# Performance work log

Hardware: AMD Instinct MI355X
Metric: run time of the kernel (lower is better)

## Reference

```python
import jax, jax.numpy as jnp
import numpy as np

N = 50000   # nodes
E = 800000  # edges (avg degree 16)
D = 128     # node feature dim
DE = 16     # edge feature dim
H = 128     # MLP hidden dim
MSG_IN = 2 * D + DE + 1  # src feat + dst feat + edge feat + squared distance


def setup_inputs() -> dict:
    key = jax.random.key(0)
    ks = jax.random.split(key, 10)
    def wmat(k, shp):
        return jax.random.normal(k, shp, jnp.float32) * 0.05
    return {
        "f": jax.random.normal(ks[0], (N, D), jnp.float32),
        "x": jax.random.normal(ks[1], (N, 3), jnp.float32),
        "w": jax.random.normal(ks[2], (E, DE), jnp.float32),
        "src": jax.random.randint(ks[3], (E,), 0, N),
        "dst": jax.random.randint(ks[4], (E,), 0, N),
        "Wm1": wmat(ks[5], (MSG_IN, H)), "bm1": jnp.zeros((H,), jnp.float32),
        "Wm2": wmat(ks[6], (H, D)),      "bm2": jnp.zeros((D,), jnp.float32),
        "Wu1": wmat(ks[7], (D, H)),      "bu1": jnp.zeros((H,), jnp.float32),
        "Wu2": wmat(ks[8], (H, D)),      "bu2": jnp.zeros((D,), jnp.float32),
    }


def reference(f, x, w, src, dst, Wm1, bm1, Wm2, bm2, Wu1, bu1, Wu2, bu2):
    # message: gather endpoint features, squared distance, concat, MLP  [E, D]
    sqd = jnp.sum((x[src] - x[dst]) ** 2, axis=-1, keepdims=True)  # [E, 1]
    msg_in = jnp.concatenate([f[src], f[dst], w, sqd], axis=-1)    # [E, MSG_IN]
    m = jnp.dot(jax.nn.relu(jnp.dot(msg_in, Wm1) + bm1), Wm2) + bm2  # [E, D]
    # reduce: sum messages at destination nodes (DGL fn.sum)
    m_sum = jax.ops.segment_sum(m, dst, num_segments=N)             # [N, D]
    # update: node MLP on m_sum + f
    h = m_sum + f
    f_new = jnp.dot(jax.nn.relu(jnp.dot(h, Wu1) + bu1), Wu2) + bu2  # [N, D]
    return f_new
```

## Files before the change

kernel.cpp:

```cpp
#include <hip/hip_runtime.h>
#include <hip/hip_fp8.h>

#define D 128
#define HD 128
#define DE 16
#define MSG_IN 273
#define EB 64
#define NT 256
#define KP1 288
#define NCH2 4
#define NB 32
#define HID_PAD 132
#define CH8 (4 * EB * 64)
#define LDS1 (4 * EB * 64 + EB * 32)
#define OB 8192
#define OC 24576

typedef __attribute__((ext_vector_type(8))) short short8v;
typedef __attribute__((ext_vector_type(4))) float f32x4;
typedef unsigned short ushort_t;
typedef unsigned char uchar_t;

#define GLOAD_LDS16(gp, lp) \
    __builtin_amdgcn_global_load_lds((const __attribute__((address_space(1))) unsigned int*)(gp), \
                                     (__attribute__((address_space(3))) unsigned int*)(lp), 16, 0, 0)

__device__ __forceinline__ unsigned short f2bf(float v) {
    unsigned int u = __builtin_bit_cast(unsigned int, v);
    u += 0x7fffu + ((u >> 16) & 1u);
    return (unsigned short)(u >> 16);
}
__device__ __forceinline__ float bf2f(ushort_t u) {
    return __builtin_bit_cast(float, (unsigned int)u << 16);
}
__device__ __forceinline__ unsigned int cvt_pk_bf16(float lo, float hi) {
    unsigned int r;
    asm("v_cvt_pk_bf16_f32 %0, %1, %2" : "=v"(r) : "v"(lo), "v"(hi));
    return r;
}
__device__ __forceinline__ uchar_t f8e(float v) {
    __hip_fp8_e4m3 t(v);
    return (uchar_t)t.__x;
}
__device__ __forceinline__ float f8d(unsigned b) {
    unsigned t = ((b & 0x7fu) << 20) | ((b & 0x80u) << 24);
    return __builtin_bit_cast(float, t) * 0x1p120f;
}

__global__ void fused_pre_kernel(const float* __restrict__ Wm1, const float* __restrict__ Wm2,
                                 const float* __restrict__ Wu1, const float* __restrict__ Wu2,
                                 ushort_t* __restrict__ W1p, ushort_t* __restrict__ W2p,
                                 ushort_t* __restrict__ Wu1p, ushort_t* __restrict__ Wu2p,
                                 const float* __restrict__ w, ushort_t* __restrict__ wbf,
                                 const int* __restrict__ dst, int* __restrict__ cnt,
                                 int nw8, int E) {
    const int gid    = blockIdx.x * 256 + threadIdx.x;
    const int stride = gridDim.x * 256;
    const int rp1 = 128 * KP1;
    const int rp2 = rp1 + HD * D;
    const int rp_elems = rp2 + 2 * HD * D;
    for (int i = gid; i < rp_elems; i += stride) {
        if (i < rp1) {
            int n = i / KP1, k = i % KP1;
            W1p[i] = f2bf((k < MSG_IN) ? Wm1[(size_t)k * HD + n] : 0.f);
        } else if (i < rp2) {
            int i2 = i - rp1;
            int n = i2 / HD, k = i2 % HD;
            W2p[i2] = f2bf(Wm2[(size_t)k * D + n]);
        } else {
            int i2 = (i - rp2);
            const bool second = i2 >= HD * D;
            if (second) i2 -= HD * D;
            int n = i2 / HD, k = i2 % HD;
            if (second) Wu2p[i2] = f2bf(Wu2[(size_t)k * D + n]);
            else        Wu1p[i2] = f2bf(Wu1[(size_t)k * HD + n]);
        }
    }
    for (int i = gid; i < nw8; i += stride) {
        float4 v0 = *(const float4*)(w + (size_t)i * 8);
        float4 v1 = *(const float4*)(w + (size_t)i * 8 + 4);
        union { ushort_t us[8]; short8v v; } pk;
        pk.us[0] = f2bf(v0.x); pk.us[1] = f2bf(v0.y);
        pk.us[2] = f2bf(v0.z); pk.us[3] = f2bf(v0.w);
        pk.us[4] = f2bf(v1.x); pk.us[5] = f2bf(v1.y);
        pk.us[6] = f2bf(v1.z); pk.us[7] = f2bf(v1.w);
        *(short8v*)(wbf + (size_t)i * 8) = pk.v;
    }
    for (int i = gid; i < E; i += stride) atomicAdd(&cnt[dst[i]], 1);
}

__global__ __launch_bounds__(1024) void scan_kernel(const int* __restrict__ cnt,
                                                    int* __restrict__ roff,
                                                    int* __restrict__ cursor, int Nn) {
    __shared__ int wsum[16];
    const int t = threadIdx.x, l = t & 63, wid = t >> 6;
    int running = 0;
    for (int base = 0; base < Nn; base += 4096) {
        const int i0 = base + t * 4;
        int v0 = 0, v1 = 0, v2 = 0, v3 = 0;
        if (i0 + 3 < Nn) {
            int4 v = *(const int4*)(cnt + i0);
            v0 = v.x; v1 = v.y; v2 = v.z; v3 = v.w;
        } else {
            if (i0 + 0 < Nn) v0 = cnt[i0 + 0];
            if (i0 + 1 < Nn) v1 = cnt[i0 + 1];
            if (i0 + 2 < Nn) v2 = cnt[i0 + 2];
        }
        const int vsum = v0 + v1 + v2 + v3;
        int s = vsum;
        #pragma unroll
        for (int off = 1; off < 64; off <<= 1) {
            int u = __shfl_up(s, off, 64);
            if (l >= off) s += u;
        }
        if (l == 63) wsum[wid] = s;
        __syncthreads();
        if (wid == 0 && l < 16) {
            int xv = wsum[l];
            #pragma unroll
            for (int off = 1; off < 16; off <<= 1) {
                int u = __shfl_up(xv, off, 64);
                if (l >= off) xv += u;
            }
            wsum[l] = xv;
        }
        __syncthreads();
        const int prev  = (wid > 0) ? wsum[wid - 1] : 0;
        const int total = wsum[15];
        int ex = running + prev + (s - vsum);
        if (i0 + 0 < Nn) { roff[i0 + 0] = ex; cursor[i0 + 0] = ex; } ex += v0;
        if (i0 + 1 < Nn) { roff[i0 + 1] = ex; cursor[i0 + 1] = ex; } ex += v1;
        if (i0 + 2 < Nn) { roff[i0 + 2] = ex; cursor[i0 + 2] = ex; } ex += v2;
        if (i0 + 3 < Nn) { roff[i0 + 3] = ex; cursor[i0 + 3] = ex; }
        running += total;
        __syncthreads();
    }
}

__global__ void scatter_kernel(const int* __restrict__ dst, int* cursor,
                               const int* __restrict__ roff, const int* __restrict__ cnt,
                               int* __restrict__ perm, int* __restrict__ sdst,
                               float* __restrict__ mh, int E, int Nn) {
    const int gid    = blockIdx.x * 256 + threadIdx.x;
    const int stride = gridDim.x * 256;
    for (int i = gid; i < E; i += stride) {
        int d = dst[i];
        int s = atomicAdd(&cursor[d], 1);
        perm[s] = i;
        sdst[s] = d;
    }
    for (int n = gid; n < Nn; n += stride) {
        const int c = cnt[n];
        const int r = roff[n];
        const bool need0 = (c == 0) || (r / EB != (r + c - 1) / EB);
        if (need0) {
            float4 z = {0.f, 0.f, 0.f, 0.f};
            float* p = mh + (size_t)n * D;
            #pragma unroll
            for (int k = 0; k < 32; ++k) *(float4*)(p + k * 4) = z;
        }
    }
}

__global__ __launch_bounds__(NT, 4) void ab_kernel(
    const float* __restrict__ f,
    const ushort_t* __restrict__ W1p,
    uchar_t* __restrict__ Af, ushort_t* __restrict__ Bf16, int Nn)
{
    __shared__ __align__(16) ushort_t lds[2 * 64 * 64];

    const int t    = threadIdx.x;
    const int lane = t & 63;
    const int wv   = t >> 6;
    const int col  = lane & 15;
    const int g    = lane >> 4;
    const int n0   = blockIdx.x * 64;

    #pragma unroll
    for (int it = 0; it < 4; ++it) {
        const int gidx = it * 256 + t;
        const int row  = gidx >> 4;
        const int gr   = gidx & 15;
        const int pair = gr >> 3, s = gr & 7;
        const int sP   = s ^ (row & 7);
        const int gn   = min(n0 + row, Nn - 1);
        const size_t off = (size_t)gn * D + gr * 8;
        float4 v0 = *(const float4*)(f + off);
        float4 v1 = *(const float4*)(f + off + 4);
        union { ushort_t us[8]; short8v v; } pk;
        pk.us[0] = f2bf(v0.x); pk.us[1] = f2bf(v0.y);
        pk.us[2] = f2bf(v0.z); pk.us[3] = f2bf(v0.w);
        pk.us[4] = f2bf(v1.x); pk.us[5] = f2bf(v1.y);
        pk.us[6] = f2bf(v1.z); pk.us[7] = f2bf(v1.w);
        *(short8v*)&lds[(pair * 64 + row) * 64 + sP * 8] = pk.v;
    }
    __syncthreads();

    const bool even = (col & 1) == 0;
    #pragma unroll
    for (int half = 0; half < 2; ++half) {
        f32x4 acc[4][2];
        #pragma unroll
        for (int rt = 0; rt < 4; ++rt) {
            acc[rt][0] = (f32x4){0.f, 0.f, 0.f, 0.f};
            acc[rt][1] = (f32x4){0.f, 0.f, 0.f, 0.f};
        }
        const int kbase = half * 128;
        #pragma unroll
        for (int c = 0; c < 4; ++c) {
            short8v b0 = *(const short8v*)&W1p[(size_t)(wv * 32 + col) * KP1 + kbase + c * 32 + g * 8];
            short8v b1 = *(const short8v*)&W1p[(size_t)(wv * 32 + 16 + col) * KP1 + kbase + c * 32 + g * 8];
            short8v a[4];
            #pragma unroll
            for (int rt = 0; rt < 4; ++rt) {
                const int row = rt * 16 + col;
                const int sP = (((c & 1) << 2) + g) ^ (row & 7);
                a[rt] = *(const short8v*)&lds[((c >> 1) * 64 + row) * 64 + sP * 8];
            }
            #pragma unroll
            for (int rt = 0; rt < 4; ++rt) {
                acc[rt][0] = __builtin_amdgcn_mfma_f32_16x16x32_bf16(a[rt], b0, acc[rt][0], 0, 0, 0);
                acc[rt][1] = __builtin_amdgcn_mfma_f32_16x16x32_bf16(a[rt], b1, acc[rt][1], 0, 0, 0);
            }
        }
        #pragma unroll
        for (int rt = 0; rt < 4; ++rt)
            #pragma unroll
            for (int j = 0; j < 2; ++j)
                #pragma unroll
                for (int r = 0; r < 4; ++r) {
                    const int row = rt * 16 + g * 4 + r;
                    const int gn = n0 + row;
                    float v  = acc[rt][j][r];
                    float vn = __shfl_xor(v, 1, 64);
                    if (even && gn < Nn) {
                        const int ca = wv * 32 + j * 16 + col;
                        if (half == 0) {
                            ushort_t pk = (ushort_t)f8e(v) | ((ushort_t)f8e(vn) << 8);
                            *(ushort_t*)(Af + (size_t)gn * D + ca) = pk;
                        } else {
                            *(unsigned int*)(Bf16 + (size_t)gn * D + ca) = cvt_pk_bf16(v, vn);
                        }
                    }
                }
    }
}

__global__ __launch_bounds__(NT, 4) void edge_lin_kernel(
    const uchar_t* __restrict__ Af, const ushort_t* __restrict__ Bf16,
    const float* __restrict__ x, const ushort_t* __restrict__ wbf,
    const int* __restrict__ src,
    const int* __restrict__ perm, const int* __restrict__ sdst,
    const ushort_t* __restrict__ W1p, const float* __restrict__ bm1,
    float* __restrict__ mh, int E)
{
    __shared__ __align__(16) uchar_t lds8[28672];
    __shared__ int s_rid[EB];
    __shared__ int s_dgs[EB];

    const int t    = threadIdx.x;
    const int lane = t & 63;
    const int wv   = t >> 6;
    const int e0   = blockIdx.x * EB;
    const int nvalid = min(EB, E - e0);

    const int myd  = (e0 + lane < E) ? sdst[e0 + lane] : -1;
    const int prevd = (e0 > 0) ? sdst[e0 - 1] : -2;
    const int nextd = (e0 + EB < E) ? sdst[e0 + EB] : -2;

    const int dprev_l = __shfl_up(myd, 1, 64);
    const bool head = (lane == 0) || (myd != dprev_l);
    const unsigned long long mask = __ballot(head && (lane < nvalid));
    const unsigned long long le = (lane == 63) ? ~0ull : ((1ull << (lane + 1)) - 1ull);
    const int rid = (int)__popcll(mask & le) - 1;
    const int ndist = (int)__popcll(mask);
    s_rid[lane] = (rid < 0) ? 0 : rid;
    if (head && lane < nvalid) s_dgs[rid] = myd;

    {
        const int el8 = lane >> 3;
        const int s   = lane & 7;
        const int sl  = s ^ el8;
        const int slA = min(e0 + wv * 16 + el8,     E - 1);
        const int slB = min(e0 + wv * 16 + 8 + el8, E - 1);
        const int nsA = src[perm[slA]];
        const int nsB = src[perm[slB]];
        GLOAD_LDS16(Af + (size_t)nsA * D + sl * 16, &lds8[(wv * 16    ) * 128]);
        GLOAD_LDS16(Af + (size_t)nsB * D + sl * 16, &lds8[(wv * 16 + 8) * 128]);
    }
    {
        const int ntask = ndist * 16;
        for (int idx = t; idx < ntask; idx += NT) {
            const int rowr = idx >> 4;
            const int gr   = idx & 15;
            const int dg   = s_dgs[rowr];
            uint4 v = *(const uint4*)(Bf16 + (size_t)dg * D + gr * 8);
            const int phys = gr ^ (rowr & 15);
            *(uint4*)&lds8[OB + rowr * 256 + phys * 16] = v;
        }
    }
    {
        const int el = lane >> 2, q = lane & 3;
        const int qp = q ^ (el & 3);
        const int slot = e0 + wv * 16 + el;
        const bool ok = slot < E;
        const int sc = min(slot, E - 1);
        const int ge = perm[sc];
        union { ushort_t us[8]; short8v v; } pk;
        #pragma unroll
        for (int j = 0; j < 8; ++j) pk.us[j] = 0;
        if (ok) {
            if (q < 2) {
                pk.v = *(const short8v*)(wbf + (size_t)ge * DE + q * 8);
            } else if (q == 2) {
                const int ns = src[ge], nd = sdst[sc];
                float dx = x[ns*3+0] - x[nd*3+0];
                float dy = x[ns*3+1] - x[nd*3+1];
                float dz = x[ns*3+2] - x[nd*3+2];
                pk.us[0] = f2bf(dx*dx + dy*dy + dz*dz);
            }
        }
        *(short8v*)&lds8[OC + (wv * 16 + el) * 64 + qp * 16] = pk.v;
    }

    const int col = lane & 15;
    const int g   = lane >> 4;

    short8v bc0 = *(const short8v*)&W1p[(size_t)(wv * 32 + col) * KP1 + 256 + g * 8];
    short8v bc1 = *(const short8v*)&W1p[(size_t)(wv * 32 + 16 + col) * KP1 + 256 + g * 8];

    __syncthreads();

    f32x4 acc[4][2];
    {
        float bv0 = bm1[wv * 32 + col];
        float bv1 = bm1[wv * 32 + 16 + col];
        #pragma unroll
        for (int rt = 0; rt < 4; ++rt) {
            acc[rt][0] = (f32x4){bv0, bv0, bv0, bv0};
            acc[rt][1] = (f32x4){bv1, bv1, bv1, bv1};
        }
    }
    #pragma unroll
    for (int rt = 0; rt < 4; ++rt) {
        const int row = rt * 16 + col;
        const int sP8 = g ^ (row & 3);
        short8v a = *(const short8v*)&lds8[OC + row * 64 + sP8 * 16];
        acc[rt][0] = __builtin_amdgcn_mfma_f32_16x16x32_bf16(a, bc0, acc[rt][0], 0, 0, 0);
        acc[rt][1] = __builtin_amdgcn_mfma_f32_16x16x32_bf16(a, bc1, acc[rt][1], 0, 0, 0);
    }

    float h[4][2][4];
    #pragma unroll
    for (int rt = 0; rt < 4; ++rt) {
        #pragma unroll
        for (int r = 0; r < 4; ++r) {
            const int row = rt * 16 + g * 4 + r;
            const int rd  = s_rid[row];
            #pragma unroll
            for (int j = 0; j < 2; ++j) {
                const int ca = wv * 32 + j * 16 + col;
                const uchar_t ab = lds8[row * 128 + (((ca >> 4) ^ (row & 7)) << 4) + (ca & 15)];
                const ushort_t bb = *(const ushort_t*)&lds8[OB + rd * 256 + (((ca >> 3) ^ (rd & 15)) << 4) + (ca & 7) * 2];
                h[rt][j][r] = fmaxf(acc[rt][j][r] + f8d(ab) + bf2f(bb), 0.f);
            }
        }
    }

    float qs[4][2];
    #pragma unroll
    for (int rt = 0; rt < 4; ++rt) {
        qs[rt][0] = (h[rt][0][0] + h[rt][0][1]) + (h[rt][0][2] + h[rt][0][3]);
        qs[rt][1] = (h[rt][1][0] + h[rt][1][1]) + (h[rt][1][2] + h[rt][1][3]);
    }
    unsigned long long rem = mask;
    while (rem) {
        const int beg = (int)__builtin_ctzll(rem);
        rem &= rem - 1;
        const int end = rem ? (int)__builtin_ctzll(rem) : nvalid;
        const int dg  = __shfl(myd, beg, 64);

        float s0 = 0.f, s1 = 0.f;
        #pragma unroll
        for (int rt = 0; rt < 4; ++rt) {
            const int qb = rt * 16 + g * 4;
            const int lo = max(qb, beg);
            const int hi = min(qb + 4, end);
            if (lo < hi) {
                if (lo == qb && hi == qb + 4) {
                    s0 += qs[rt][0]; s1 += qs[rt][1];
                } else {
                    #pragma unroll
                    for (int r = 0; r < 4; ++r) {
                        const int sl = qb + r;
                        if (sl >= beg && sl < end) {
                            s0 += h[rt][0][r]; s1 += h[rt][1][r];
                        }
                    }
                }
            }
        }
        s0 += __shfl_xor(s0, 16, 64); s0 += __shfl_xor(s0, 32, 64);
        s1 += __shfl_xor(s1, 16, 64); s1 += __shfl_xor(s1, 32, 64);
        if (g == 0) {
            const bool bnd = (beg == 0 && dg == prevd) || (end == nvalid && dg == nextd);
            float* p = mh + (size_t)dg * D + wv * 32 + col;
            if (bnd) { atomicAdd(p, s0); atomicAdd(p + 16, s1); }
            else     { p[0] = s0; p[16] = s1; }
        }
    }
}

__global__ __launch_bounds__(NT, 4) void node_fused_kernel(
    const float* __restrict__ f, const float* __restrict__ mh,
    const int* __restrict__ cnt,
    const ushort_t* __restrict__ W2p, const float* __restrict__ bm2,
    const ushort_t* __restrict__ Wu1p, const float* __restrict__ bu1,
    const ushort_t* __restrict__ Wu2p, const float* __restrict__ bu2,
    float* __restrict__ out, int Nn)
{
    __shared__ __align__(16) ushort_t lds[2 * 64 * 64];
    __shared__ int s_cnt[64];

    const int t    = threadIdx.x;
    const int lane = t & 63;
    const int wv   = t >> 6;
    const int col  = lane & 15;
    const int g    = lane >> 4;
    const int n0   = blockIdx.x * 64;

    if (t < 64) s_cnt[t] = (n0 + t < Nn) ? cnt[n0 + t] : 0;

    #pragma unroll
    for (int it = 0; it < 4; ++it) {
        const int gidx = it * 256 + t;
        const int row  = gidx >> 4;
        const int gr   = gidx & 15;
        const int pair = gr >> 3, s = gr & 7;
        const int sP   = s ^ (row & 7);
        const int gn   = n0 + row;
        union { ushort_t us[8]; short8v v; } pk;
        if (gn < Nn) {
            const size_t off = (size_t)gn * D + gr * 8;
            float4 m0 = *(const float4*)(mh + off);
            float4 m1 = *(const float4*)(mh + off + 4);
            pk.us[0] = f2bf(m0.x); pk.us[1] = f2bf(m0.y);
            pk.us[2] = f2bf(m0.z); pk.us[3] = f2bf(m0.w);
            pk.us[4] = f2bf(m1.x); pk.us[5] = f2bf(m1.y);
            pk.us[6] = f2bf(m1.z); pk.us[7] = f2bf(m1.w);
        } else {
            #pragma unroll
            for (int j = 0; j < 8; ++j) pk.us[j] = 0;
        }
        *(short8v*)&lds[(pair * 64 + row) * 64 + sP * 8] = pk.v;
    }
    __syncthreads();

    f32x4 acc[4][2];
    {
        const float bv0 = bm2[wv * 32 + col];
        const float bv1 = bm2[wv * 32 + 16 + col];
        #pragma unroll
        for (int rt = 0; rt < 4; ++rt)
            #pragma unroll
            for (int r = 0; r < 4; ++r) {
                const float cn = (float)s_cnt[rt * 16 + g * 4 + r];
                acc[rt][0][r] = cn * bv0;
                acc[rt][1][r] = cn * bv1;
            }
    }
    #pragma unroll
    for (int c = 0; c < 4; ++c) {
        short8v b0 = *(const short8v*)&W2p[(size_t)(wv * 32 + col) * HD + c * 32 + g * 8];
        short8v b1 = *(const short8v*)&W2p[(size_t)(wv * 32 + 16 + col) * HD + c * 32 + g * 8];
        short8v a[4];
        #pragma unroll
        for (int rt = 0; rt < 4; ++rt) {
            const int row = rt * 16 + col;
            const int sP = (((c & 1) << 2) + g) ^ (row & 7);
            a[rt] = *(const short8v*)&lds[((c >> 1) * 64 + row) * 64 + sP * 8];
        }
        #pragma unroll
        for (int rt = 0; rt < 4; ++rt) {
            acc[rt][0] = __builtin_amdgcn_mfma_f32_16x16x32_bf16(a[rt], b0, acc[rt][0], 0, 0, 0);
            acc[rt][1] = __builtin_amdgcn_mfma_f32_16x16x32_bf16(a[rt], b1, acc[rt][1], 0, 0, 0);
        }
    }
    __syncthreads();

    const int ph = wv >> 1;
    #pragma unroll
    for (int rt = 0; rt < 4; ++rt)
        #pragma unroll
        for (int r = 0; r < 4; ++r) {
            const int row = rt * 16 + g * 4 + r;
            const int gn = n0 + row;
            #pragma unroll
            for (int j = 0; j < 2; ++j) {
                const int ca = wv * 32 + j * 16 + col;
                float v = 0.f;
                if (gn < Nn) v = acc[rt][j][r] + f[(size_t)gn * D + ca];
                unsigned int pk2 = cvt_pk_bf16(v, v);
                const int sH = (((wv & 1) << 2) + j * 2 + (col >> 3)) ^ (row & 7);
                lds[(ph * 64 + row) * 64 + sH * 8 + (col & 7)] = (ushort_t)pk2;
            }
        }
    __syncthreads();

    const size_t wrow0 = (size_t)(wv * 32 + col) * HD;
    const size_t wrow1 = (size_t)(wv * 32 + 16 + col) * HD;
    f32x4 acc1[4][2];
    {
        float bv0 = bu1[wv * 32 + col];
        float bv1 = bu1[wv * 32 + 16 + col];
        #pragma unroll
        for (int rt = 0; rt < 4; ++rt) {
            acc1[rt][0] = (f32x4){bv0, bv0, bv0, bv0};
            acc1[rt][1] = (f32x4){bv1, bv1, bv1, bv1};
        }
    }
    #pragma unroll
    for (int c = 0; c < 4; ++c) {
        short8v b0 = *(const short8v*)&Wu1p[wrow0 + c * 32 + g * 8];
        short8v b1 = *(const short8v*)&Wu1p[wrow1 + c * 32 + g * 8];
        short8v a[4];
        #pragma unroll
        for (int rt = 0; rt < 4; ++rt) {
            const int row = rt * 16 + col;
            const int sP = (((c & 1) << 2) + g) ^ (row & 7);
            a[rt] = *(const short8v*)&lds[((c >> 1) * 64 + row) * 64 + sP * 8];
        }
        #pragma unroll
        for (int rt = 0; rt < 4; ++rt) {
            acc1[rt][0] = __builtin_amdgcn_mfma_f32_16x16x32_bf16(a[rt], b0, acc1[rt][0], 0, 0, 0);
            acc1[rt][1] = __builtin_amdgcn_mfma_f32_16x16x32_bf16(a[rt], b1, acc1[rt][1], 0, 0, 0);
        }
    }
    __syncthreads();

    #pragma unroll
    for (int rt = 0; rt < 4; ++rt)
        #pragma unroll
        for (int j = 0; j < 2; ++j)
            #pragma unroll
            for (int r = 0; r < 4; ++r) {
                const int row = rt * 16 + g * 4 + r;
                float v = fmaxf(acc1[rt][j][r], 0.f);
                unsigned int pk2 = cvt_pk_bf16(v, v);
                const int sH = (((wv & 1) << 2) + j * 2 + (col >> 3)) ^ (row & 7);
                lds[(ph * 64 + row) * 64 + sH * 8 + (col & 7)] = (ushort_t)pk2;
            }
    __syncthreads();

    f32x4 acc2[4][2];
    {
        float bv0 = bu2[wv * 32 + col];
        float bv1 = bu2[wv * 32 + 16 + col];
        #pragma unroll
        for (int rt = 0; rt < 4; ++rt) {
            acc2[rt][0] = (f32x4){bv0, bv0, bv0, bv0};
            acc2[rt][1] = (f32x4){bv1, bv1, bv1, bv1};
        }
    }
    #pragma unroll
    for (int c = 0; c < 4; ++c) {
        short8v b0 = *(const short8v*)&Wu2p[wrow0 + c * 32 + g * 8];
        short8v b1 = *(const short8v*)&Wu2p[wrow1 + c * 32 + g * 8];
        short8v a[4];
        #pragma unroll
        for (int rt = 0; rt < 4; ++rt) {
            const int row = rt * 16 + col;
            const int sP = (((c & 1) << 2) + g) ^ (row & 7);
            a[rt] = *(const short8v*)&lds[((c >> 1) * 64 + row) * 64 + sP * 8];
        }
        #pragma unroll
        for (int rt = 0; rt < 4; ++rt) {
            acc2[rt][0] = __builtin_amdgcn_mfma_f32_16x16x32_bf16(a[rt], b0, acc2[rt][0], 0, 0, 0);
            acc2[rt][1] = __builtin_amdgcn_mfma_f32_16x16x32_bf16(a[rt], b1, acc2[rt][1], 0, 0, 0);
        }
    }

    #pragma unroll
    for (int rt = 0; rt < 4; ++rt)
        #pragma unroll
        for (int r = 0; r < 4; ++r) {
            const int row = rt * 16 + g * 4 + r;
            const int gn = n0 + row;
            if (gn < Nn) {
                out[(size_t)gn * D + wv * 32 + col]      = acc2[rt][0][r];
                out[(size_t)gn * D + wv * 32 + 16 + col] = acc2[rt][1][r];
            }
        }
}


__global__ void repack_kernel(const float* __restrict__ Wm1, const float* __restrict__ Wm2,
                              ushort_t* __restrict__ W1p, ushort_t* __restrict__ W2p) {
    int idx = blockIdx.x * 256 + threadIdx.x;
    const int n1 = 128 * KP1;
    if (idx < n1) {
        int n = idx / KP1, k = idx % KP1;
        W1p[idx] = f2bf((k < MSG_IN) ? Wm1[(size_t)k * HD + n] : 0.f);
    } else {
        int i2 = idx - n1;
        if (i2 < HD * D) {
            int n = i2 / HD, k = i2 % HD;
            W2p[i2] = f2bf(Wm2[(size_t)k * D + n]);
        }
    }
}

__global__ void fconv_kernel(const float* __restrict__ f, ushort_t* __restrict__ fb, int n8) {
    int i = blockIdx.x * 256 + threadIdx.x;
    if (i < n8) {
        float4 v0 = *(const float4*)(f + (size_t)i * 8);
        float4 v1 = *(const float4*)(f + (size_t)i * 8 + 4);
        union { ushort_t us[8]; short8v v; } pk;
        pk.us[0] = f2bf(v0.x); pk.us[1] = f2bf(v0.y);
        pk.us[2] = f2bf(v0.z); pk.us[3] = f2bf(v0.w);
        pk.us[4] = f2bf(v1.x); pk.us[5] = f2bf(v1.y);
        pk.us[6] = f2bf(v1.z); pk.us[7] = f2bf(v1.w);
        *(short8v*)(fb + (size_t)i * 8) = pk.v;
    }
}

__global__ __launch_bounds__(NT, 4) void edge_mfma_kernel(
    const ushort_t* __restrict__ fbf, const float* __restrict__ x,
    const float* __restrict__ w, const int* __restrict__ src,
    const int* __restrict__ dst,
    const ushort_t* __restrict__ W1p, const float* __restrict__ bm1,
    const ushort_t* __restrict__ W2p, const float* __restrict__ bm2,
    ushort_t* msum, int E)
{
    __shared__ __align__(16) ushort_t lds[LDS1];
    __shared__ int s_dst[EB];

    const int t    = threadIdx.x;
    const int lane = t & 63;
    const int wv   = t >> 6;
    const int e0   = blockIdx.x * EB;

    if (t < EB) s_dst[t] = (e0 + t < E) ? dst[e0 + t] : 0;
    {
        const int el8 = lane >> 3;
        const int s   = lane & 7;
        const int sl  = s ^ el8;
        const int geA = min(e0 + wv * 16 + el8,     E - 1);
        const int geB = min(e0 + wv * 16 + 8 + el8, E - 1);
        const int nsA = src[geA], ndA = dst[geA];
        const int nsB = src[geB], ndB = dst[geB];
        #pragma unroll
        for (int p = 0; p < 4; ++p) {
            const int n0 = (p < 2) ? nsA : ndA;
            const int n1 = (p < 2) ? nsB : ndB;
            const ushort_t* g0 = fbf + (size_t)n0 * D + (p & 1) * 64 + sl * 8;
            const ushort_t* g1 = fbf + (size_t)n1 * D + (p & 1) * 64 + sl * 8;
            GLOAD_LDS16(g0, &lds[(p * EB + wv * 16    ) * 64]);
            GLOAD_LDS16(g1, &lds[(p * EB + wv * 16 + 8) * 64]);
        }
    }
    {
        const int el = lane >> 2, q = lane & 3;
        const int qp = q ^ (el & 3);
        const int ge = e0 + wv * 16 + el;
        const bool ok = ge < E;
        const int gc = min(ge, E - 1);
        union { ushort_t us[8]; short8v v; } pk;
        #pragma unroll
        for (int j = 0; j < 8; ++j) pk.us[j] = 0;
        if (ok) {
            if (q < 2) {
                float4 w0 = *(const float4*)(w + (size_t)gc * DE + q * 8);
                float4 w1 = *(const float4*)(w + (size_t)gc * DE + q * 8 + 4);
                pk.us[0] = f2bf(w0.x); pk.us[1] = f2bf(w0.y);
                pk.us[2] = f2bf(w0.z); pk.us[3] = f2bf(w0.w);
                pk.us[4] = f2bf(w1.x); pk.us[5] = f2bf(w1.y);
                pk.us[6] = f2bf(w1.z); pk.us[7] = f2bf(w1.w);
            } else if (q == 2) {
                const int ns = src[gc], nd = dst[gc];
                float dx = x[ns*3+0] - x[nd*3+0];
                float dy = x[ns*3+1] - x[nd*3+1];
                float dz = x[ns*3+2] - x[nd*3+2];
                pk.us[0] = f2bf(dx*dx + dy*dy + dz*dz);
            }
        }
        *(short8v*)&lds[CH8 + (wv * 16 + el) * 32 + qp * 8] = pk.v;
    }

    const int col = lane & 15;
    const int g   = lane >> 4;
    const size_t wrow0 = (size_t)(wv * 32 + col) * KP1;
    const size_t wrow1 = (size_t)(wv * 32 + 16 + col) * KP1;
    short8v nb0 = *(const short8v*)&W1p[wrow0 + g * 8];
    short8v nb1 = *(const short8v*)&W1p[wrow1 + g * 8];
    __syncthreads();

    f32x4 acc[4][2];
    {
        float bv0 = bm1[wv * 32 + col];
        float bv1 = bm1[wv * 32 + 16 + col];
        #pragma unroll
        for (int rt = 0; rt < 4; ++rt) {
            acc[rt][0] = (f32x4){bv0, bv0, bv0, bv0};
            acc[rt][1] = (f32x4){bv1, bv1, bv1, bv1};
        }
    }
    #pragma unroll
    for (int c = 0; c < 9; ++c) {
        short8v b0 = nb0, b1 = nb1;
        if (c + 1 < 9) {
            nb0 = *(const short8v*)&W1p[wrow0 + (c + 1) * 32 + g * 8];
            nb1 = *(const short8v*)&W1p[wrow1 + (c + 1) * 32 + g * 8];
        }
        short8v a[4];
        #pragma unroll
        for (int rt = 0; rt < 4; ++rt) {
            const int row = rt * 16 + col;
            if (c < 8) {
                const int sP = (((c & 1) << 2) + g) ^ (row & 7);
                a[rt] = *(const short8v*)&lds[((c >> 1) * EB + row) * 64 + sP * 8];
            } else {
                const int sP = g ^ (row & 3);
                a[rt] = *(const short8v*)&lds[CH8 + row * 32 + sP * 8];
            }
        }
        #pragma unroll
        for (int rt = 0; rt < 4; ++rt) {
            acc[rt][0] = __builtin_amdgcn_mfma_f32_16x16x32_bf16(a[rt], b0, acc[rt][0], 0, 0, 0);
            acc[rt][1] = __builtin_amdgcn_mfma_f32_16x16x32_bf16(a[rt], b1, acc[rt][1], 0, 0, 0);
        }
    }
    __syncthreads();

    const int ph = wv >> 1;
    #pragma unroll
    for (int rt = 0; rt < 4; ++rt)
        #pragma unroll
        for (int j = 0; j < 2; ++j)
            #pragma unroll
            for (int r = 0; r < 4; ++r) {
                const int row = rt * 16 + g * 4 + r;
                float v = fmaxf(acc[rt][j][r], 0.f);
                unsigned int pk2 = cvt_pk_bf16(v, v);
                const int sH = (((wv & 1) << 2) + j * 2 + (col >> 3)) ^ (row & 7);
                lds[(ph * EB + row) * 64 + sH * 8 + (col & 7)] = (ushort_t)pk2;
            }
    __syncthreads();

    const size_t w2r0 = (size_t)(wv * 32 + col) * HD;
    const size_t w2r1 = (size_t)(wv * 32 + 16 + col) * HD;
    short8v m0 = *(const short8v*)&W2p[w2r0 + g * 8];
    short8v m1 = *(const short8v*)&W2p[w2r1 + g * 8];
    f32x4 acc2[4][2];
    {
        float bv0 = bm2[wv * 32 + col];
        float bv1 = bm2[wv * 32 + 16 + col];
        #pragma unroll
        for (int rt = 0; rt < 4; ++rt) {
            acc2[rt][0] = (f32x4){bv0, bv0, bv0, bv0};
            acc2[rt][1] = (f32x4){bv1, bv1, bv1, bv1};
        }
    }
    #pragma unroll
    for (int c = 0; c < NCH2; ++c) {
        short8v b0 = m0, b1 = m1;
        if (c + 1 < NCH2) {
            m0 = *(const short8v*)&W2p[w2r0 + (c + 1) * 32 + g * 8];
            m1 = *(const short8v*)&W2p[w2r1 + (c + 1) * 32 + g * 8];
        }
        short8v a[4];
        #pragma unroll
        for (int rt = 0; rt < 4; ++rt) {
            const int row = rt * 16 + col;
            const int sP = (((c & 1) << 2) + g) ^ (row & 7);
            a[rt] = *(const short8v*)&lds[((c >> 1) * EB + row) * 64 + sP * 8];
        }
        #pragma unroll
        for (int rt = 0; rt < 4; ++rt) {
            acc2[rt][0] = __builtin_amdgcn_mfma_f32_16x16x32_bf16(a[rt], b0, acc2[rt][0], 0, 0, 0);
            acc2[rt][1] = __builtin_amdgcn_mfma_f32_16x16x32_bf16(a[rt], b1, acc2[rt][1], 0, 0, 0);
        }
    }

    const bool even = (col & 1) == 0;
    #pragma unroll
    for (int rt = 0; rt < 4; ++rt)
        #pragma unroll
        for (int r = 0; r < 4; ++r) {
            const int e  = rt * 16 + g * 4 + r;
            const int ge = e0 + e;
            const int dg = s_dst[e];
            #pragma unroll
            for (int j = 0; j < 2; ++j) {
                float v  = acc2[rt][j][r];
                float vn = __shfl_xor(v, 1, 64);
                if (even && ge < E) {
                    unsigned int pk2 = cvt_pk_bf16(v, vn);
                    ushort_t* p = msum + (size_t)dg * D + wv * 32 + j * 16 + col;
                    asm volatile("global_atomic_pk_add_bf16 %0, %1, off"
                                 :: "v"(p), "v"(pk2) : "memory");
                }
            }
        }
}

template<bool MB16>
__global__ __launch_bounds__(NT, 4) void node_kernel(
    const float* __restrict__ f, const void* __restrict__ msum_v,
    const float* __restrict__ Wu1, const float* __restrict__ bu1,
    const float* __restrict__ Wu2, const float* __restrict__ bu2,
    float* out, int Nn)
{
    __shared__ __align__(16) float hin[NB][HID_PAD];
    __shared__ __align__(16) float hid[NB][HID_PAD];
    const int t  = threadIdx.x;
    const int n0 = blockIdx.x * NB;
    const int nn = min(NB, Nn - n0);

    {
        #pragma unroll
        for (int it = 0; it < 4; ++it) {
            const int idx = it * 1024 + t * 4;
            const int e   = idx >> 7;
            const int cb  = idx & 127;
            if (e < nn) {
                const size_t off = (size_t)(n0 + e) * D + cb;
                float4 mv;
                if (MB16) {
                    uint2 pk = *(const uint2*)((const ushort_t*)msum_v + off);
                    mv.x = bf2f((ushort_t)(pk.x & 0xffffu));
                    mv.y = bf2f((ushort_t)(pk.x >> 16));
                    mv.z = bf2f((ushort_t)(pk.y & 0xffffu));
                    mv.w = bf2f((ushort_t)(pk.y >> 16));
                } else {
                    mv = *(const float4*)((const float*)msum_v + off);
                }
                float4 fv = *(const float4*)&f[off];
                float4 o = {mv.x + fv.x, mv.y + fv.y, mv.z + fv.z, mv.w + fv.w};
                *(float4*)&hin[e][cb] = o;
            }
        }
    }
    __syncthreads();

    const int tc = t & 15, te2 = (t >> 4) * 2, c0 = tc * 8;
    float a1[2][8];
    #pragma unroll
    for (int c = 0; c < 8; ++c) { float bv = bu1[c0 + c]; a1[0][c] = bv; a1[1][c] = bv; }
    for (int i = 0; i < D; i += 4) {
        float m0[4], m1[4];
        *(float4*)m0 = *(const float4*)&hin[te2][i];
        *(float4*)m1 = *(const float4*)&hin[te2 + 1][i];
        #pragma unroll
        for (int r = 0; r < 4; ++r) {
            float wr[8];
            *(float4*)&wr[0] = *(const float4*)(Wu1 + (size_t)(i + r) * HD + c0);
            *(float4*)&wr[4] = *(const float4*)(Wu1 + (size_t)(i + r) * HD + c0 + 4);
            #pragma unroll
            for (int c = 0; c < 8; ++c) { a1[0][c] += m0[r]*wr[c]; a1[1][c] += m1[r]*wr[c]; }
        }
    }
    #pragma unroll
    for (int j = 0; j < 2; ++j) {
        float v[8];
        #pragma unroll
        for (int c = 0; c < 8; ++c) v[c] = fmaxf(a1[j][c], 0.f);
        *(float4*)&hid[te2 + j][c0] = *(float4*)&v[0];
        *(float4*)&hid[te2 + j][c0 + 4] = *(float4*)&v[4];
    }
    __syncthreads();
    float a2[2][8];
    #pragma unroll
    for (int c = 0; c < 8; ++c) { float bv = bu2[c0 + c]; a2[0][c] = bv; a2[1][c] = bv; }
    for (int h = 0; h < HD; h += 4) {
        float m0[4], m1[4];
        *(float4*)m0 = *(const float4*)&hid[te2][h];
        *(float4*)m1 = *(const float4*)&hid[te2 + 1][h];
        #pragma unroll
        for (int r = 0; r < 4; ++r) {
            float wr[8];
            *(float4*)&wr[0] = *(const float4*)(Wu2 + (size_t)(h + r) * D + c0);
            *(float4*)&wr[4] = *(const float4*)(Wu2 + (size_t)(h + r) * D + c0 + 4);
            #pragma unroll
            for (int c = 0; c < 8; ++c) { a2[0][c] += m0[r]*wr[c]; a2[1][c] += m1[r]*wr[c]; }
        }
    }
    #pragma unroll
    for (int j = 0; j < 2; ++j) {
        int e = te2 + j, gn = n0 + e;
        if (e < nn) {
            *(float4*)(out + (size_t)gn * D + c0) = *(float4*)&a2[j][0];
            *(float4*)(out + (size_t)gn * D + c0 + 4) = *(float4*)&a2[j][4];
        }
    }
}

extern "C" void kernel_launch(void* const* d_in, const int* in_sizes, int n_in,
                              void* d_out, int out_size, void* d_ws, size_t ws_size,
                              hipStream_t stream) {
    const float* f   = (const float*)d_in[0];
    const float* x   = (const float*)d_in[1];
    const float* w   = (const float*)d_in[2];
    const int*   src = (const int*)d_in[3];
    const int*   dst = (const int*)d_in[4];
    const float* Wm1 = (const float*)d_in[5];
    const float* bm1 = (const float*)d_in[6];
    const float* Wm2 = (const float*)d_in[7];
    const float* bm2 = (const float*)d_in[8];
    const float* Wu1 = (const float*)d_in[9];
    const float* bu1 = (const float*)d_in[10];
    const float* Wu2 = (const float*)d_in[11];
    const float* bu2 = (const float*)d_in[12];

    const int Nn = in_sizes[0] / D;
    const int E  = in_sizes[3];

    const size_t wbytes  = (size_t)(128 * KP1 + HD * D) * sizeof(ushort_t);
    const size_t wubytes = (size_t)(2 * HD * D) * sizeof(ushort_t);
    auto align512 = [](size_t v) { return (v + 511) & ~(size_t)511; };
    char* wsb = (char*)d_ws;

    size_t off = 0;
    const size_t o_w    = off; off = align512(off + wbytes);
    const size_t o_wu   = off; off = align512(off + wubytes);
    const size_t o_wbf  = off; off = align512(off + (size_t)E * DE * 2);
    const size_t o_af   = off; off = align512(off + (size_t)Nn * D);
    const size_t o_bf16 = off; off = align512(off + (size_t)Nn * D * 2);
    const size_t o_cnt  = off; off = align512(off + (size_t)Nn * 4);
    const size_t o_roff = off; off = align512(off + (size_t)Nn * 4);
    const size_t o_cur  = off; off = align512(off + (size_t)Nn * 4);
    const size_t o_perm = off; off = align512(off + (size_t)E * 4);
    const size_t o_sdst = off; off = align512(off + (size_t)E * 4);
    const size_t o_mh   = off; off = align512(off + (size_t)Nn * D * 4);
    const size_t primary_total = off;

    if (ws_size >= primary_total) {
        ushort_t* W1p  = (ushort_t*)(wsb + o_w);
        ushort_t* W2p  = W1p + 128 * KP1;
        ushort_t* Wu1p = (ushort_t*)(wsb + o_wu);
        ushort_t* Wu2p = Wu1p + HD * D;
        ushort_t* wbf  = (ushort_t*)(wsb + o_wbf);
        uchar_t*  Af   = (uchar_t*)(wsb + o_af);
        ushort_t* Bf16 = (ushort_t*)(wsb + o_bf16);
        int* cnt       = (int*)(wsb + o_cnt);
        int* roff      = (int*)(wsb + o_roff);
        int* cursor    = (int*)(wsb + o_cur);
        int* perm      = (int*)(wsb + o_perm);
        int* sdst      = (int*)(wsb + o_sdst);
        float* mh      = (float*)(wsb + o_mh);

        const int nw8 = E * DE / 8;
        const int ntiles = (E + EB - 1) / EB;
        const int nblk   = (Nn + 63) / 64;
        hipMemsetAsync(cnt, 0, (size_t)Nn * 4, stream);
        fused_pre_kernel<<<dim3(1024), dim3(256), 0, stream>>>(
            Wm1, Wm2, Wu1, Wu2, W1p, W2p, Wu1p, Wu2p, w, wbf, dst, cnt, nw8, E);
        scan_kernel<<<dim3(1), dim3(1024), 0, stream>>>(cnt, roff, cursor, Nn);
        scatter_kernel<<<dim3((E + 255) / 256), dim3(256), 0, stream>>>(
            dst, cursor, roff, cnt, perm, sdst, mh, E, Nn);
        ab_kernel<<<dim3(nblk), dim3(NT), 0, stream>>>(f, W1p, Af, Bf16, Nn);
        edge_lin_kernel<<<dim3(ntiles), dim3(NT), 0, stream>>>(
            Af, Bf16, x, wbf, src, perm, sdst, W1p, bm1, mh, E);
        node_fused_kernel<<<dim3(nblk), dim3(NT), 0, stream>>>(
            f, mh, cnt, W2p, bm2, Wu1p, bu1, Wu2p, bu2, (float*)d_out, Nn);
        return;
    }

    size_t off2 = 0;
    const size_t p_w  = off2; off2 = align512(off2 + wbytes);
    const size_t p_fb = off2; off2 = align512(off2 + (size_t)Nn * D * 2);
    const size_t p_ms = off2; off2 = align512(off2 + (size_t)Nn * D * 2);
    if (ws_size >= off2) {
        ushort_t* W1p  = (ushort_t*)(wsb + p_w);
        ushort_t* W2p  = W1p + 128 * KP1;
        ushort_t* fbf  = (ushort_t*)(wsb + p_fb);
        ushort_t* msum = (ushort_t*)(wsb + p_ms);
        const int rp_elems = 128 * KP1 + HD * D;
        hipMemsetAsync(msum, 0, (size_t)Nn * D * 2, stream);
        repack_kernel<<<dim3((rp_elems + 255) / 256), dim3(256), 0, stream>>>(Wm1, Wm2, W1p, W2p);
        const int n8 = Nn * D / 8;
        fconv_kernel<<<dim3((n8 + 255) / 256), dim3(256), 0, stream>>>(f, fbf, n8);
        edge_mfma_kernel<<<dim3((E + EB - 1) / EB), dim3(NT), 0, stream>>>(
            fbf, x, w, src, dst, W1p, bm1, W2p, bm2, msum, E);
        node_kernel<true><<<dim3((Nn + NB - 1) / NB), dim3(NT), 0, stream>>>(
            f, msum, Wu1, bu1, Wu2, bu2, (float*)d_out, Nn);
        return;
    }
}
```

Before: 261.0 us.

## Fuse edge-feature bf16 conversion into edge kernel and raise occupancy bound

Drops the pre-pass that converted the edge features w to a bf16 workspace buffer. The edge kernel now reads fp32 w directly through the permutation and converts it in registers. This removes a full write and re-read of the E x 16 buffer, but doubles the bytes of the scattered per-edge read. It also raises the edge kernel's launch-bounds occupancy hint from 4 to 5 and simplifies LDS address arithmetic in the hidden-activation epilogue, which adds register pressure risk.

Measured after the change: 254.3 us. 1.03x faster.

```diff
diff --git a/kernel.cpp b/kernel.cpp
--- a/kernel.cpp
+++ b/kernel.cpp
@@ -51,9 +51,8 @@
                                  const float* __restrict__ Wu1, const float* __restrict__ Wu2,
                                  ushort_t* __restrict__ W1p, ushort_t* __restrict__ W2p,
                                  ushort_t* __restrict__ Wu1p, ushort_t* __restrict__ Wu2p,
-                                 const float* __restrict__ w, ushort_t* __restrict__ wbf,
                                  const int* __restrict__ dst, int* __restrict__ cnt,
-                                 int nw8, int E) {
+                                 int E) {
     const int gid    = blockIdx.x * 256 + threadIdx.x;
     const int stride = gridDim.x * 256;
     const int rp1 = 128 * KP1;
@@ -76,16 +75,6 @@
             else        Wu1p[i2] = f2bf(Wu1[(size_t)k * HD + n]);
         }
     }
-    for (int i = gid; i < nw8; i += stride) {
-        float4 v0 = *(const float4*)(w + (size_t)i * 8);
-        float4 v1 = *(const float4*)(w + (size_t)i * 8 + 4);
-        union { ushort_t us[8]; short8v v; } pk;
-        pk.us[0] = f2bf(v0.x); pk.us[1] = f2bf(v0.y);
-        pk.us[2] = f2bf(v0.z); pk.us[3] = f2bf(v0.w);
-        pk.us[4] = f2bf(v1.x); pk.us[5] = f2bf(v1.y);
-        pk.us[6] = f2bf(v1.z); pk.us[7] = f2bf(v1.w);
-        *(short8v*)(wbf + (size_t)i * 8) = pk.v;
-    }
     for (int i = gid; i < E; i += stride) atomicAdd(&cnt[dst[i]], 1);
 }
 
@@ -246,9 +235,9 @@
     }
 }
 
-__global__ __launch_bounds__(NT, 4) void edge_lin_kernel(
+__global__ __launch_bounds__(NT, 5) void edge_lin_kernel(
     const uchar_t* __restrict__ Af, const ushort_t* __restrict__ Bf16,
-    const float* __restrict__ x, const ushort_t* __restrict__ wbf,
+    const float* __restrict__ x, const float* __restrict__ w,
     const int* __restrict__ src,
     const int* __restrict__ perm, const int* __restrict__ sdst,
     const ushort_t* __restrict__ W1p, const float* __restrict__ bm1,
@@ -311,7 +300,12 @@
         for (int j = 0; j < 8; ++j) pk.us[j] = 0;
         if (ok) {
             if (q < 2) {
-                pk.v = *(const short8v*)(wbf + (size_t)ge * DE + q * 8);
+                float4 w0 = *(const float4*)(w + (size_t)ge * DE + q * 8);
+                float4 w1 = *(const float4*)(w + (size_t)ge * DE + q * 8 + 4);
+                pk.us[0] = f2bf(w0.x); pk.us[1] = f2bf(w0.y);
+                pk.us[2] = f2bf(w0.z); pk.us[3] = f2bf(w0.w);
+                pk.us[4] = f2bf(w1.x); pk.us[5] = f2bf(w1.y);
+                pk.us[6] = f2bf(w1.z); pk.us[7] = f2bf(w1.w);
             } else if (q == 2) {
                 const int ns = src[ge], nd = sdst[sc];
                 float dx = x[ns*3+0] - x[nd*3+0];
@@ -351,19 +345,23 @@
     }
 
     float h[4][2][4];
+    const int cgA = 2 * wv;
+    const int cbB = 4 * wv + (col >> 3);
+    const int coB = (col & 7) * 2;
     #pragma unroll
     for (int rt = 0; rt < 4; ++rt) {
         #pragma unroll
         for (int r = 0; r < 4; ++r) {
             const int row = rt * 16 + g * 4 + r;
             const int rd  = s_rid[row];
-            #pragma unroll
-            for (int j = 0; j < 2; ++j) {
-                const int ca = wv * 32 + j * 16 + col;
-                const uchar_t ab = lds8[row * 128 + (((ca >> 4) ^ (row & 7)) << 4) + (ca & 15)];
-                const ushort_t bb = *(const ushort_t*)&lds8[OB + rd * 256 + (((ca >> 3) ^ (rd & 15)) << 4) + (ca & 7) * 2];
-                h[rt][j][r] = fmaxf(acc[rt][j][r] + f8d(ab) + bf2f(bb), 0.f);
-            }
+            const int aadr = row * 128 + ((cgA ^ (row & 7)) << 4) + col;
+            const int badr = OB + rd * 256 + ((cbB ^ (rd & 15)) << 4) + coB;
+            const uchar_t  a0 = lds8[aadr];
+            const uchar_t  a1 = lds8[aadr ^ 16];
+            const ushort_t b0 = *(const ushort_t*)&lds8[badr];
+            const ushort_t b1 = *(const ushort_t*)&lds8[badr ^ 32];
+            h[rt][0][r] = fmaxf(acc[rt][0][r] + f8d(a0) + bf2f(b0), 0.f);
+            h[rt][1][r] = fmaxf(acc[rt][1][r] + f8d(a1) + bf2f(b1), 0.f);
         }
     }
 
@@ -923,7 +921,6 @@
     size_t off = 0;
     const size_t o_w    = off; off = align512(off + wbytes);
     const size_t o_wu   = off; off = align512(off + wubytes);
-    const size_t o_wbf  = off; off = align512(off + (size_t)E * DE * 2);
     const size_t o_af   = off; off = align512(off + (size_t)Nn * D);
     const size_t o_bf16 = off; off = align512(off + (size_t)Nn * D * 2);
     const size_t o_cnt  = off; off = align512(off + (size_t)Nn * 4);
@@ -939,7 +936,6 @@
         ushort_t* W2p  = W1p + 128 * KP1;
         ushort_t* Wu1p = (ushort_t*)(wsb + o_wu);
         ushort_t* Wu2p = Wu1p + HD * D;
-        ushort_t* wbf  = (ushort_t*)(wsb + o_wbf);
         uchar_t*  Af   = (uchar_t*)(wsb + o_af);
         ushort_t* Bf16 = (ushort_t*)(wsb + o_bf16);
         int* cnt       = (int*)(wsb + o_cnt);
@@ -949,18 +945,17 @@
         int* sdst      = (int*)(wsb + o_sdst);
         float* mh      = (float*)(wsb + o_mh);
 
-        const int nw8 = E * DE / 8;
         const int ntiles = (E + EB - 1) / EB;
         const int nblk   = (Nn + 63) / 64;
         hipMemsetAsync(cnt, 0, (size_t)Nn * 4, stream);
         fused_pre_kernel<<<dim3(1024), dim3(256), 0, stream>>>(
-            Wm1, Wm2, Wu1, Wu2, W1p, W2p, Wu1p, Wu2p, w, wbf, dst, cnt, nw8, E);
+            Wm1, Wm2, Wu1, Wu2, W1p, W2p, Wu1p, Wu2p, dst, cnt, E);
         scan_kernel<<<dim3(1), dim3(1024), 0, stream>>>(cnt, roff, cursor, Nn);
         scatter_kernel<<<dim3((E + 255) / 256), dim3(256), 0, stream>>>(
             dst, cursor, roff, cnt, perm, sdst, mh, E, Nn);
         ab_kernel<<<dim3(nblk), dim3(NT), 0, stream>>>(f, W1p, Af, Bf16, Nn);
         edge_lin_kernel<<<dim3(ntiles), dim3(NT), 0, stream>>>(
-            Af, Bf16, x, wbf, src, perm, sdst, W1p, bm1, mh, E);
+            Af, Bf16, x, w, src, perm, sdst, W1p, bm1, mh, E);
         node_fused_kernel<<<dim3(nblk), dim3(NT), 0, stream>>>(
             f, mh, cnt, W2p, bm2, Wu1p, bu1, Wu2p, bu2, (float*)d_out, Nn);
         return;
```
